# Kernel tuning notes

Hardware: AMD Instinct MI355X
Metric: run time of the kernel (lower is better)

The kernel has to match this reference:

```python
import jax, jax.numpy as jnp
import numpy as np

N_NODES = 100000
N_EDGES = 1000000
D_FEAT = 64          # per-node embedding dim
IN_FEATS = 2 * D_FEAT  # concat(src, dst)
HID = 128


def setup_inputs() -> dict:
    key = jax.random.key(0)
    ks = jax.random.split(key, 12)
    zi = jax.random.normal(ks[0], (N_NODES, D_FEAT), dtype=jnp.float32)
    zj = jax.random.normal(ks[1], (N_NODES, D_FEAT), dtype=jnp.float32)
    zn = jax.random.normal(ks[2], (N_NODES, D_FEAT), dtype=jnp.float32)
    pos_src = jax.random.randint(ks[3], (N_EDGES,), 0, N_NODES)
    pos_dst = jax.random.randint(ks[4], (N_EDGES,), 0, N_NODES)
    neg_src = jax.random.randint(ks[5], (N_EDGES,), 0, N_NODES)
    neg_dst = jax.random.randint(ks[6], (N_EDGES,), 0, N_NODES)
    # MLP params (nn.Linear style: y = x @ W.T + b)
    s1 = 1.0 / np.sqrt(IN_FEATS)
    s3 = 1.0 / np.sqrt(HID)
    W1 = jax.random.uniform(ks[7], (HID, IN_FEATS), jnp.float32, -s1, s1)
    b1 = jax.random.uniform(ks[8], (HID,), jnp.float32, -s1, s1)
    W3 = jax.random.uniform(ks[9], (1, HID), jnp.float32, -s3, s3)
    b3 = jax.random.uniform(ks[10], (1,), jnp.float32, -s3, s3)
    return {"zi": zi, "zj": zj, "zn": zn, "W1": W1, "b1": b1, "W3": W3,
            "b3": b3, "pos_src": pos_src, "pos_dst": pos_dst,
            "neg_src": neg_src, "neg_dst": neg_dst}


def _lp(raw, W1, b1, W3, b3):
    # Link_Prediction with n_layers=2, dropout=0: linear-relu-linear-sigmoid
    hid = jax.nn.relu(raw @ W1.T + b1)      # [E, HID]
    return jax.nn.sigmoid(hid @ W3.T + b3)  # [E, 1]


def reference(zi, zj, zn, W1, b1, W3, b3, pos_src, pos_dst, neg_src, neg_dst):
    # pos graph: gather src/dst node embeddings per edge, concat -> MLP
    raw_pos = jnp.concatenate([zi[pos_src], zj[pos_dst]], axis=1)  # [E, 2*D]
    pos_score = _lp(raw_pos, W1, b1, W3, b3)
    # NOTE: source bug — neg score is computed from the POS raw features
    # (pos_graph.edata['raw']); the neg gather/concat is dead code, so we
    # faithfully score raw_pos again.
    neg_score = _lp(raw_pos, W1, b1, W3, b3)
    return pos_score, neg_score
```

## Files before the change

### kernel.cpp

```cpp
#include <hip/hip_runtime.h>
#include <hip/hip_fp8.h>

typedef float    f32x16 __attribute__((ext_vector_type(16)));
typedef _Float16 f16x8  __attribute__((ext_vector_type(8)));
typedef long     i64;

#define NWAVES 4
#define TPW 4
#define TILES_PER_BLOCK (NWAVES * TPW)

__device__ __forceinline__ uint32_t enc4_fp8(float a, float b, float c, float d) {
#if __has_builtin(__builtin_amdgcn_cvt_pk_fp8_f32)
    int w = __builtin_amdgcn_cvt_pk_fp8_f32(a, b, 0, false);
    w     = __builtin_amdgcn_cvt_pk_fp8_f32(c, d, w, true);
    return (uint32_t)w;
#else
    __hip_fp8_e4m3 e0(a), e1(b), e2(c), e3(d);
    return (uint32_t)e0.__x | ((uint32_t)e1.__x << 8) |
           ((uint32_t)e2.__x << 16) | ((uint32_t)e3.__x << 24);
#endif
}

__device__ __forceinline__ void dec4_fp8f(uint32_t w, float* o) {
#if __has_builtin(__builtin_amdgcn_cvt_pk_f32_fp8)
    const auto f01 = __builtin_amdgcn_cvt_pk_f32_fp8((int)w, false);
    const auto f23 = __builtin_amdgcn_cvt_pk_f32_fp8((int)w, true);
    o[0] = f01[0]; o[1] = f01[1]; o[2] = f23[0]; o[3] = f23[1];
#else
    #pragma unroll
    for (int j = 0; j < 4; ++j) {
        __hip_fp8_e4m3 t; t.__x = (unsigned char)(w >> (8 * j));
        o[j] = (float)t;
    }
#endif
}

__device__ __forceinline__ i64 mk64(uint32_t lo, uint32_t hi) {
    return (i64)(((unsigned long long)hi << 32) | (unsigned long long)lo);
}

__global__ __launch_bounds__(256) void prep_fp8(
    const float* __restrict__ zi, const float* __restrict__ zj,
    uint2* __restrict__ zif8, uint2* __restrict__ zjf8, const int nChunkPer)
{
    const int stride = gridDim.x * blockDim.x;
    for (int c = blockIdx.x * blockDim.x + threadIdx.x; c < 2 * nChunkPer; c += stride) {
        const float* s;
        uint2* d;
        int cc;
        if (c < nChunkPer) { cc = c; s = zi + (size_t)cc * 8; d = zif8 + cc; }
        else { cc = c - nChunkPer; s = zj + (size_t)cc * 8; d = zjf8 + cc; }
        const float4 a0 = *reinterpret_cast<const float4*>(s);
        const float4 a1 = *reinterpret_cast<const float4*>(s + 4);
        uint2 w;
        w.x = enc4_fp8(a0.x, a0.y, a0.z, a0.w);
        w.y = enc4_fp8(a1.x, a1.y, a1.z, a1.w);
        *d = w;
    }
}

__global__ __launch_bounds__(256) void prep_w1(
    const float* __restrict__ W1, uint4* __restrict__ w1pack)
{
    const int c = blockIdx.x * blockDim.x + threadIdx.x;
    if (c >= 2048) return;
    const int n  = c >> 4, q = c & 15;
    const int kk = q >> 1, lq = q & 1;
    const int kbase = (kk < 4) ? (lq * 32 + kk * 8) : (64 + lq * 32 + (kk - 4) * 8);
    const float* w = W1 + n * 128 + kbase;
    const float4 w0 = *reinterpret_cast<const float4*>(w);
    const float4 w1 = *reinterpret_cast<const float4*>(w + 4);
    const uint32_t h0 = enc4_fp8(w0.x, w0.y, w0.z, w0.w);
    const uint32_t h1 = enc4_fp8(w1.x, w1.y, w1.z, w1.w);
    float d0[4], d1[4];
    dec4_fp8f(h0, d0);
    dec4_fp8f(h1, d1);
    const uint32_t r0 = enc4_fp8((w0.x - d0[0]) * 16.0f, (w0.y - d0[1]) * 16.0f,
                                 (w0.z - d0[2]) * 16.0f, (w0.w - d0[3]) * 16.0f);
    const uint32_t r1 = enc4_fp8((w1.x - d1[0]) * 16.0f, (w1.y - d1[1]) * 16.0f,
                                 (w1.z - d1[2]) * 16.0f, (w1.w - d1[3]) * 16.0f);
    uint4 o; o.x = h0; o.y = h1; o.z = r0; o.w = r1;
    w1pack[c] = o;
}

template<bool FP8>
__global__ __launch_bounds__(256) void graphlp_mfma(
    const float* __restrict__ zi, const float* __restrict__ zj,
    const unsigned char* __restrict__ zif8, const unsigned char* __restrict__ zjf8,
    const uint4* __restrict__ w1pack,
    const float* __restrict__ W1, const float* __restrict__ b1p,
    const float* __restrict__ W3, const float* __restrict__ b3p,
    const int* __restrict__ psrc, const int* __restrict__ pdst,
    float* __restrict__ out, const int nEdges, const int nTiles)
{
    __shared__ uint4 w1s[2048];
    char* lds = reinterpret_cast<char*>(w1s);
    const int tid = threadIdx.x;

    if constexpr (FP8) {
        #pragma unroll
        for (int i = 0; i < 8; ++i) {
            const int ch = tid + i * 256;
            const int n  = ch >> 4;
            const int q  = ch & 15;
            const uint4 v = w1pack[ch];
            const int off = n * 256 + ((q * 16) ^ ((n & 7) << 4));
            *reinterpret_cast<uint4*>(lds + off) = v;
        }
    } else {
        #pragma unroll
        for (int i = 0; i < 8; ++i) {
            const int ch  = tid + i * 256;
            const int row = ch >> 4;
            const int kg  = ch & 15;
            const float* s = W1 + row * 128 + kg * 8;
            const float4 a0 = *reinterpret_cast<const float4*>(s);
            const float4 a1 = *reinterpret_cast<const float4*>(s + 4);
            f16x8 v;
            v[0]=(_Float16)a0.x; v[1]=(_Float16)a0.y; v[2]=(_Float16)a0.z; v[3]=(_Float16)a0.w;
            v[4]=(_Float16)a1.x; v[5]=(_Float16)a1.y; v[6]=(_Float16)a1.z; v[7]=(_Float16)a1.w;
            const int off = row * 256 + ((kg * 16) ^ ((row & 7) << 4));
            *reinterpret_cast<f16x8*>(lds + off) = v;
        }
    }
    __syncthreads();

    const int lane = tid & 63;
    const int wav  = tid >> 6;
    const int lr   = lane & 31;
    const int lq   = lane >> 5;

    float b1v[4], w3v[4];
    #pragma unroll
    for (int nb = 0; nb < 4; ++nb) {
        b1v[nb] = b1p[nb * 32 + lr];
        w3v[nb] = W3[nb * 32 + lr];
    }
    const float b3 = b3p[0];

    int si = 0, di = 0;
    {
        const int g0 = blockIdx.x * TILES_PER_BLOCK + wav;
        if (g0 < nTiles) {
            const int e = min(g0 * 32 + lr, nEdges - 1);
            si = psrc[e]; di = pdst[e];
        }
    }

    for (int t = 0; t < TPW; ++t) {
        const int g = blockIdx.x * TILES_PER_BLOCK + t * NWAVES + wav;
        if (g >= nTiles) break;

        int si_n = 0, di_n = 0;
        if (t + 1 < TPW) {
            const int gn = g + NWAVES;
            if (gn < nTiles) {
                const int en = min(gn * 32 + lr, nEdges - 1);
                si_n = psrc[en]; di_n = pdst[en];
            }
        }

        float pr[16];
        #pragma unroll
        for (int r = 0; r < 16; ++r) pr[r] = 0.0f;

        if constexpr (FP8) {
            const unsigned char* __restrict__ sp = zif8 + (size_t)si * 64;
            const unsigned char* __restrict__ dp = zjf8 + (size_t)di * 64;
            const uint4 as0 = *reinterpret_cast<const uint4*>(sp + lq * 32);
            const uint4 as1 = *reinterpret_cast<const uint4*>(sp + lq * 32 + 16);
            const uint4 ad0 = *reinterpret_cast<const uint4*>(dp + lq * 32);
            const uint4 ad1 = *reinterpret_cast<const uint4*>(dp + lq * 32 + 16);
            i64 aop[8];
            aop[0] = mk64(as0.x, as0.y); aop[1] = mk64(as0.z, as0.w);
            aop[2] = mk64(as1.x, as1.y); aop[3] = mk64(as1.z, as1.w);
            aop[4] = mk64(ad0.x, ad0.y); aop[5] = mk64(ad0.z, ad0.w);
            aop[6] = mk64(ad1.x, ad1.y); aop[7] = mk64(ad1.z, ad1.w);

            #pragma unroll
            for (int nb = 0; nb < 4; ++nb) {
                const float bb = b1v[nb];
                f32x16 acc, accr;
                #pragma unroll
                for (int r = 0; r < 16; ++r) { acc[r] = bb; accr[r] = 0.0f; }
                const int n   = nb * 32 + lr;
                const int nsw = (n & 7) << 4;
                const int nbase = n * 256;
                __builtin_amdgcn_s_setprio(1);
                #pragma unroll
                for (int kk = 0; kk < 8; ++kk) {
                    const int off = nbase + (((kk * 2 + lq) * 16) ^ nsw);
                    const uint4 w = *reinterpret_cast<const uint4*>(lds + off);
                    acc  = __builtin_amdgcn_mfma_f32_32x32x16_fp8_fp8(
                               aop[kk], mk64(w.x, w.y), acc,  0, 0, 0);
                    accr = __builtin_amdgcn_mfma_f32_32x32x16_fp8_fp8(
                               aop[kk], mk64(w.z, w.w), accr, 0, 0, 0);
                }
                __builtin_amdgcn_s_setprio(0);
                const float ww = w3v[nb];
                #pragma unroll
                for (int r = 0; r < 16; ++r) {
                    const float h = fmaf(accr[r], 0.0625f, acc[r]);
                    pr[r] = fmaf(fmaxf(h, 0.0f), ww, pr[r]);
                }
            }
        } else {
            f16x8 afrag[8];
            const float* __restrict__ sp = zi + (size_t)si * 64;
            const float* __restrict__ dp = zj + (size_t)di * 64;
            #pragma unroll
            for (int kk = 0; kk < 8; ++kk) {
                const int kb = kk * 16 + lq * 8;
                const float* p = (kk < 4) ? (sp + kb) : (dp + kb - 64);
                const float4 a0 = *reinterpret_cast<const float4*>(p);
                const float4 a1 = *reinterpret_cast<const float4*>(p + 4);
                f16x8 v;
                v[0]=(_Float16)a0.x; v[1]=(_Float16)a0.y; v[2]=(_Float16)a0.z; v[3]=(_Float16)a0.w;
                v[4]=(_Float16)a1.x; v[5]=(_Float16)a1.y; v[6]=(_Float16)a1.z; v[7]=(_Float16)a1.w;
                afrag[kk] = v;
            }
            #pragma unroll
            for (int nbp = 0; nbp < 2; ++nbp) {
                const float bb0 = b1v[2*nbp], bb1 = b1v[2*nbp + 1];
                f32x16 acc0, acc1;
                #pragma unroll
                for (int r = 0; r < 16; ++r) { acc0[r] = bb0; acc1[r] = bb1; }
                const int n0 = (2*nbp)     * 32 + lr;
                const int n1 = (2*nbp + 1) * 32 + lr;
                #pragma unroll
                for (int kk = 0; kk < 8; ++kk) {
                    const int kx = kk * 32 + lq * 16;
                    const f16x8 bf0 = *reinterpret_cast<const f16x8*>(
                        lds + n0 * 256 + (kx ^ ((n0 & 7) << 4)));
                    const f16x8 bf1 = *reinterpret_cast<const f16x8*>(
                        lds + n1 * 256 + (kx ^ ((n1 & 7) << 4)));
                    acc0 = __builtin_amdgcn_mfma_f32_32x32x16_f16(afrag[kk], bf0, acc0, 0, 0, 0);
                    acc1 = __builtin_amdgcn_mfma_f32_32x32x16_f16(afrag[kk], bf1, acc1, 0, 0, 0);
                }
                const float ww0 = w3v[2*nbp], ww1 = w3v[2*nbp + 1];
                #pragma unroll
                for (int r = 0; r < 16; ++r) {
                    pr[r] = fmaf(fmaxf(acc0[r], 0.0f), ww0, pr[r]);
                    pr[r] = fmaf(fmaxf(acc1[r], 0.0f), ww1, pr[r]);
                }
            }
        }

        float p8[8];
        #pragma unroll
        for (int r = 0; r < 8; ++r) {
            const float lo = pr[r], hi = pr[r + 8];
            const float sent = (lane & 1) ? lo : hi;
            const float got  = __shfl_xor(sent, 1);
            p8[r] = ((lane & 1) ? hi : lo) + got;
        }
        float p4[4];
        #pragma unroll
        for (int r = 0; r < 4; ++r) {
            const float lo = p8[r], hi = p8[r + 4];
            const float sent = (lane & 2) ? lo : hi;
            const float got  = __shfl_xor(sent, 2);
            p4[r] = ((lane & 2) ? hi : lo) + got;
        }
        float p2[2];
        #pragma unroll
        for (int r = 0; r < 2; ++r) {
            const float lo = p4[r], hi = p4[r + 2];
            const float sent = (lane & 4) ? lo : hi;
            const float got  = __shfl_xor(sent, 4);
            p2[r] = ((lane & 4) ? hi : lo) + got;
        }
        float p1;
        {
            const float lo = p2[0], hi = p2[1];
            const float sent = (lane & 8) ? lo : hi;
            const float got  = __shfl_xor(sent, 8);
            p1 = ((lane & 8) ? hi : lo) + got;
        }
        p1 += __shfl_xor(p1, 16);

        const int rid = 8 * (lane & 1) + 4 * ((lane >> 1) & 1)
                      + 2 * ((lane >> 2) & 1) + ((lane >> 3) & 1);
        const int m  = (rid & 3) + 8 * (rid >> 2) + 4 * lq;
        const int eo = g * 32 + m;
        if (eo < nEdges) {
            const float sc = 1.0f / (1.0f + __expf(-(p1 + b3)));
            if (lane & 16) out[nEdges + eo] = sc;
            else           out[eo] = sc;
        }

        si = si_n; di = di_n;
    }
}

extern "C" void kernel_launch(void* const* d_in, const int* in_sizes, int n_in,
                              void* d_out, int out_size, void* d_ws, size_t ws_size,
                              hipStream_t stream)
{
    const float* zi = (const float*)d_in[0];
    const float* zj = (const float*)d_in[1];
    const float* W1 = (const float*)d_in[3];
    const float* b1 = (const float*)d_in[4];
    const float* W3 = (const float*)d_in[5];
    const float* b3 = (const float*)d_in[6];
    const int* psrc = (const int*)d_in[7];
    const int* pdst = (const int*)d_in[8];
    float* out = (float*)d_out;

    const int nEdges = in_sizes[7];
    const int nNodesI = in_sizes[0] / 64;
    const int nNodesJ = in_sizes[1] / 64;
    const int nTiles = (nEdges + 31) / 32;
    const int nBlocks = (nTiles + TILES_PER_BLOCK - 1) / TILES_PER_BLOCK;

    const size_t bytesI = (size_t)nNodesI * 64;
    const size_t bytesJ = (size_t)nNodesJ * 64;
    const size_t bytesW = 2048 * 16;
    const bool useF8 = (ws_size >= bytesI + bytesJ + bytesW);

    if (useF8) {
        unsigned char* zif8 = (unsigned char*)d_ws;
        unsigned char* zjf8 = (unsigned char*)d_ws + bytesI;
        uint4* w1pack = (uint4*)((unsigned char*)d_ws + bytesI + bytesJ);
        const int nChunkPer = nNodesI * 64 / 8;
        hipLaunchKernelGGL(prep_fp8, dim3(2048), dim3(256), 0, stream,
                           zi, zj, (uint2*)zif8, (uint2*)zjf8, nChunkPer);
        hipLaunchKernelGGL(prep_w1, dim3(8), dim3(256), 0, stream, W1, w1pack);
        hipLaunchKernelGGL((graphlp_mfma<true>), dim3(nBlocks), dim3(256), 0, stream,
                           zi, zj, zif8, zjf8, w1pack, W1, b1, W3, b3, psrc, pdst,
                           out, nEdges, nTiles);
    } else {
        hipLaunchKernelGGL((graphlp_mfma<false>), dim3(nBlocks), dim3(256), 0, stream,
                           zi, zj, (const unsigned char*)nullptr, (const unsigned char*)nullptr,
                           (const uint4*)nullptr, W1, b1, W3, b3, psrc, pdst,
                           out, nEdges, nTiles);
    }
}
```

Baseline: 71.67 us.

## Double-buffer FP8 embedding gathers into LDS via async global_load_lds

In the FP8 path, all edge indices for the wave's tiles are loaded up front. Node-embedding rows are then gathered with global_load_lds directly into a per-wave double-buffered LDS staging area, so the next tile's gather overlaps the current tile's MFMA work, with explicit vmcnt waits. Out-of-range tiles are clamped rather than skipped, and writes go unconditionally to clamped indices. LDS use grows from 32KB to 64KB per block, which may reduce occupancy.

Result: slower. 78.47 us (+9.5%).

```diff
diff --git a/kernel.cpp b/kernel.cpp
--- a/kernel.cpp
+++ b/kernel.cpp
@@ -8,6 +8,7 @@
 #define NWAVES 4
 #define TPW 4
 #define TILES_PER_BLOCK (NWAVES * TPW)
+#define W1_LDS 32768
 
 __device__ __forceinline__ uint32_t enc4_fp8(float a, float b, float c, float d) {
 #if __has_builtin(__builtin_amdgcn_cvt_pk_fp8_f32)
@@ -37,6 +38,12 @@
 
 __device__ __forceinline__ i64 mk64(uint32_t lo, uint32_t hi) {
     return (i64)(((unsigned long long)hi << 32) | (unsigned long long)lo);
+}
+
+__device__ __forceinline__ void gl_lds16(const void* g, void* l) {
+    __builtin_amdgcn_global_load_lds(
+        (const __attribute__((address_space(1))) void*)g,
+        (__attribute__((address_space(3))) void*)l, 16, 0, 0);
 }
 
 __global__ __launch_bounds__(256) void prep_fp8(
@@ -93,8 +100,8 @@
     const int* __restrict__ psrc, const int* __restrict__ pdst,
     float* __restrict__ out, const int nEdges, const int nTiles)
 {
-    __shared__ uint4 w1s[2048];
-    char* lds = reinterpret_cast<char*>(w1s);
+    __shared__ char ldsbuf[65536];
+    char* lds = ldsbuf;
     const int tid = threadIdx.x;
 
     if constexpr (FP8) {
@@ -138,44 +145,61 @@
     }
     const float b3 = b3p[0];
 
-    int si = 0, di = 0;
-    {
-        const int g0 = blockIdx.x * TILES_PER_BLOCK + wav;
-        if (g0 < nTiles) {
-            const int e = min(g0 * 32 + lr, nEdges - 1);
-            si = psrc[e]; di = pdst[e];
-        }
-    }
-
-    for (int t = 0; t < TPW; ++t) {
-        const int g = blockIdx.x * TILES_PER_BLOCK + t * NWAVES + wav;
-        if (g >= nTiles) break;
-
-        int si_n = 0, di_n = 0;
-        if (t + 1 < TPW) {
-            const int gn = g + NWAVES;
-            if (gn < nTiles) {
-                const int en = min(gn * 32 + lr, nEdges - 1);
-                si_n = psrc[en]; di_n = pdst[en];
-            }
-        }
-
-        float pr[16];
+    const int nT1 = nTiles - 1;
+    const int gb  = blockIdx.x * TILES_PER_BLOCK + wav;
+
+    if constexpr (FP8) {
+        int sia[TPW], dia[TPW];
         #pragma unroll
-        for (int r = 0; r < 16; ++r) pr[r] = 0.0f;
-
-        if constexpr (FP8) {
-            const unsigned char* __restrict__ sp = zif8 + (size_t)si * 64;
-            const unsigned char* __restrict__ dp = zjf8 + (size_t)di * 64;
-            const uint4 as0 = *reinterpret_cast<const uint4*>(sp + lq * 32);
-            const uint4 as1 = *reinterpret_cast<const uint4*>(sp + lq * 32 + 16);
-            const uint4 ad0 = *reinterpret_cast<const uint4*>(dp + lq * 32);
-            const uint4 ad1 = *reinterpret_cast<const uint4*>(dp + lq * 32 + 16);
+        for (int t = 0; t < TPW; ++t) {
+            const int gt = min(gb + t * NWAVES, nT1);
+            const int et = min(gt * 32 + lr, nEdges - 1);
+            sia[t] = psrc[et];
+            dia[t] = pdst[et];
+        }
+        char* stage = ldsbuf + W1_LDS + wav * 8192;
+        {
+            const unsigned char* sp = zif8 + (size_t)sia[0] * 64 + lq * 16;
+            const unsigned char* dp = zjf8 + (size_t)dia[0] * 64 + lq * 16;
+            gl_lds16(sp,      stage);
+            gl_lds16(sp + 32, stage + 1024);
+            gl_lds16(dp,      stage + 2048);
+            gl_lds16(dp + 32, stage + 3072);
+        }
+
+        #pragma unroll
+        for (int t = 0; t < TPW; ++t) {
+            const int g = min(gb + t * NWAVES, nT1);
+
+            {
+                const int tn = (t + 1 < TPW) ? (t + 1) : t;
+                char* dst = stage + ((t + 1) & 1) * 4096;
+                const unsigned char* sp = zif8 + (size_t)sia[tn] * 64 + lq * 16;
+                const unsigned char* dp = zjf8 + (size_t)dia[tn] * 64 + lq * 16;
+                gl_lds16(sp,      dst);
+                gl_lds16(sp + 32, dst + 1024);
+                gl_lds16(dp,      dst + 2048);
+                gl_lds16(dp + 32, dst + 3072);
+            }
+
+            if (t == 0) asm volatile("s_waitcnt vmcnt(4)" ::: "memory");
+            else        asm volatile("s_waitcnt vmcnt(5)" ::: "memory");
+            __builtin_amdgcn_sched_barrier(0);
+
+            const char* rb = stage + (t & 1) * 4096 + lq * 1024 + lr * 16;
+            const uint4 as0 = *reinterpret_cast<const uint4*>(rb);
+            const uint4 as1 = *reinterpret_cast<const uint4*>(rb + 512);
+            const uint4 ad0 = *reinterpret_cast<const uint4*>(rb + 2048);
+            const uint4 ad1 = *reinterpret_cast<const uint4*>(rb + 2560);
             i64 aop[8];
             aop[0] = mk64(as0.x, as0.y); aop[1] = mk64(as0.z, as0.w);
             aop[2] = mk64(as1.x, as1.y); aop[3] = mk64(as1.z, as1.w);
             aop[4] = mk64(ad0.x, ad0.y); aop[5] = mk64(ad0.z, ad0.w);
             aop[6] = mk64(ad1.x, ad1.y); aop[7] = mk64(ad1.z, ad1.w);
+
+            float pr[16];
+            #pragma unroll
+            for (int r = 0; r < 16; ++r) pr[r] = 0.0f;
 
             #pragma unroll
             for (int nb = 0; nb < 4; ++nb) {
@@ -204,7 +228,67 @@
                     pr[r] = fmaf(fmaxf(h, 0.0f), ww, pr[r]);
                 }
             }
-        } else {
+
+            float p8[8];
+            #pragma unroll
+            for (int r = 0; r < 8; ++r) {
+                const float lo = pr[r], hi = pr[r + 8];
+                const float sent = (lane & 1) ? lo : hi;
+                const float got  = __shfl_xor(sent, 1);
+                p8[r] = ((lane & 1) ? hi : lo) + got;
+            }
+            float p4[4];
+            #pragma unroll
+            for (int r = 0; r < 4; ++r) {
+                const float lo = p8[r], hi = p8[r + 4];
+                const float sent = (lane & 2) ? lo : hi;
+                const float got  = __shfl_xor(sent, 2);
+                p4[r] = ((lane & 2) ? hi : lo) + got;
+            }
+            float p2[2];
+            #pragma unroll
+            for (int r = 0; r < 2; ++r) {
+                const float lo = p4[r], hi = p4[r + 2];
+                const float sent = (lane & 4) ? lo : hi;
+                const float got  = __shfl_xor(sent, 4);
+                p2[r] = ((lane & 4) ? hi : lo) + got;
+            }
+            float p1;
+            {
+                const float lo = p2[0], hi = p2[1];
+                const float sent = (lane & 8) ? lo : hi;
+                const float got  = __shfl_xor(sent, 8);
+                p1 = ((lane & 8) ? hi : lo) + got;
+            }
+            p1 += __shfl_xor(p1, 16);
+
+            const int rid = 8 * (lane & 1) + 4 * ((lane >> 1) & 1)
+                          + 2 * ((lane >> 2) & 1) + ((lane >> 3) & 1);
+            const int m  = (rid & 3) + 8 * (rid >> 2) + 4 * lq;
+            const int eoc = min(g * 32 + m, nEdges - 1);
+            const float sc = 1.0f / (1.0f + __expf(-(p1 + b3)));
+            out[(lane & 16) ? (nEdges + eoc) : eoc] = sc;
+        }
+    } else {
+        int si = 0, di = 0;
+        {
+            const int g0 = gb;
+            if (g0 < nTiles) {
+                const int e = min(g0 * 32 + lr, nEdges - 1);
+                si = psrc[e]; di = pdst[e];
+            }
+        }
+        for (int t = 0; t < TPW; ++t) {
+            const int g = gb + t * NWAVES;
+            if (g >= nTiles) break;
+            int si_n = 0, di_n = 0;
+            if (t + 1 < TPW) {
+                const int gn = g + NWAVES;
+                if (gn < nTiles) {
+                    const int en = min(gn * 32 + lr, nEdges - 1);
+                    si_n = psrc[en]; di_n = pdst[en];
+                }
+            }
             f16x8 afrag[8];
             const float* __restrict__ sp = zi + (size_t)si * 64;
             const float* __restrict__ dp = zj + (size_t)di * 64;
@@ -219,6 +303,9 @@
                 v[4]=(_Float16)a1.x; v[5]=(_Float16)a1.y; v[6]=(_Float16)a1.z; v[7]=(_Float16)a1.w;
                 afrag[kk] = v;
             }
+            float pr[16];
+            #pragma unroll
+            for (int r = 0; r < 16; ++r) pr[r] = 0.0f;
             #pragma unroll
             for (int nbp = 0; nbp < 2; ++nbp) {
                 const float bb0 = b1v[2*nbp], bb1 = b1v[2*nbp + 1];
@@ -244,52 +331,49 @@
                     pr[r] = fmaf(fmaxf(acc1[r], 0.0f), ww1, pr[r]);
                 }
             }
-        }
-
-        float p8[8];
-        #pragma unroll
-        for (int r = 0; r < 8; ++r) {
-            const float lo = pr[r], hi = pr[r + 8];
-            const float sent = (lane & 1) ? lo : hi;
-            const float got  = __shfl_xor(sent, 1);
-            p8[r] = ((lane & 1) ? hi : lo) + got;
-        }
-        float p4[4];
-        #pragma unroll
-        for (int r = 0; r < 4; ++r) {
-            const float lo = p8[r], hi = p8[r + 4];
-            const float sent = (lane & 2) ? lo : hi;
-            const float got  = __shfl_xor(sent, 2);
-            p4[r] = ((lane & 2) ? hi : lo) + got;
-        }
-        float p2[2];
-        #pragma unroll
-        for (int r = 0; r < 2; ++r) {
-            const float lo = p4[r], hi = p4[r + 2];
-            const float sent = (lane & 4) ? lo : hi;
-            const float got  = __shfl_xor(sent, 4);
-            p2[r] = ((lane & 4) ? hi : lo) + got;
-        }
-        float p1;
-        {
-            const float lo = p2[0], hi = p2[1];
-            const float sent = (lane & 8) ? lo : hi;
-            const float got  = __shfl_xor(sent, 8);
-            p1 = ((lane & 8) ? hi : lo) + got;
-        }
-        p1 += __shfl_xor(p1, 16);
-
-        const int rid = 8 * (lane & 1) + 4 * ((lane >> 1) & 1)
-                      + 2 * ((lane >> 2) & 1) + ((lane >> 3) & 1);
-        const int m  = (rid & 3) + 8 * (rid >> 2) + 4 * lq;
-        const int eo = g * 32 + m;
-        if (eo < nEdges) {
-            const float sc = 1.0f / (1.0f + __expf(-(p1 + b3)));
-            if (lane & 16) out[nEdges + eo] = sc;
-            else           out[eo] = sc;
-        }
-
-        si = si_n; di = di_n;
+            float p8[8];
+            #pragma unroll
+            for (int r = 0; r < 8; ++r) {
+                const float lo = pr[r], hi = pr[r + 8];
+                const float sent = (lane & 1) ? lo : hi;
+                const float got  = __shfl_xor(sent, 1);
+                p8[r] = ((lane & 1) ? hi : lo) + got;
+            }
+            float p4[4];
+            #pragma unroll
+            for (int r = 0; r < 4; ++r) {
+                const float lo = p8[r], hi = p8[r + 4];
+                const float sent = (lane & 2) ? lo : hi;
+                const float got  = __shfl_xor(sent, 2);
+                p4[r] = ((lane & 2) ? hi : lo) + got;
+            }
+            float p2[2];
+            #pragma unroll
+            for (int r = 0; r < 2; ++r) {
+                const float lo = p4[r], hi = p4[r + 2];
+                const float sent = (lane & 4) ? lo : hi;
+                const float got  = __shfl_xor(sent, 4);
+                p2[r] = ((lane & 4) ? hi : lo) + got;
+            }
+            float p1;
+            {
+                const float lo = p2[0], hi = p2[1];
+                const float sent = (lane & 8) ? lo : hi;
+                const float got  = __shfl_xor(sent, 8);
+                p1 = ((lane & 8) ? hi : lo) + got;
+            }
+            p1 += __shfl_xor(p1, 16);
+            const int rid = 8 * (lane & 1) + 4 * ((lane >> 1) & 1)
+                          + 2 * ((lane >> 2) & 1) + ((lane >> 3) & 1);
+            const int m  = (rid & 3) + 8 * (rid >> 2) + 4 * lq;
+            const int eo = g * 32 + m;
+            if (eo < nEdges) {
+                const float sc = 1.0f / (1.0f + __expf(-(p1 + b3)));
+                if (lane & 16) out[nEdges + eo] = sc;
+                else           out[eo] = sc;
+            }
+            si = si_n; di = di_n;
+        }
     }
 }
 
```
